# Kernel optimization log

Hardware: AMD Instinct MI355X
Metric: run time of the kernel (lower is better)

## Reference

```python
import jax, jax.numpy as jnp
import numpy as np

N = 200000   # nodes
E = 3200000  # edges
B = 1024     # graphs in batch
A = 10       # num_actions
IN, C, ED = 9, 64, 1
NEG_SLOPE = 0.2


def _xavier(k, shape):
    lim = (6.0 / (shape[0] + shape[1])) ** 0.5
    return jax.random.uniform(k, shape, jnp.float32, -lim, lim)


def setup_inputs() -> dict:
    key = jax.random.key(0)
    ks = jax.random.split(key, 24)
    x = jax.random.normal(ks[0], (N, IN), jnp.float32)
    edge_index = jax.random.randint(ks[1], (2, E), 0, N, dtype=jnp.int64)
    edge_attr = jax.random.normal(ks[2], (E, ED), jnp.float32)
    agent_state = jax.random.normal(ks[3], (B, 34), jnp.float32)
    pool_batch = jnp.sort(jax.random.randint(ks[4], (N,), 0, B, dtype=jnp.int64))
    return {
        "x": x, "edge_index": edge_index, "edge_attr": edge_attr,
        "agent_state": agent_state, "pool_batch": pool_batch,
        # GATConv params (heads=1): lin (no bias), lin_edge (no bias), att vectors, bias
        "W_gat": _xavier(ks[5], (IN, C)),
        "att_src": jax.random.normal(ks[6], (C,), jnp.float32) * 0.1,
        "att_dst": jax.random.normal(ks[7], (C,), jnp.float32) * 0.1,
        "W_edge": _xavier(ks[8], (ED, C)),
        "att_edge": jax.random.normal(ks[9], (C,), jnp.float32) * 0.1,
        "b_gat": jnp.zeros((C,), jnp.float32),
        # fc_input1: Linear(64,128)
        "W1": _xavier(ks[10], (C, 128)), "b1": jnp.zeros((128,), jnp.float32),
        # fc_input2: Linear(34,64)
        "W2": _xavier(ks[11], (34, 64)), "b2": jnp.zeros((64,), jnp.float32),
        # fc_output: Linear(192,128), Linear(128,A)
        "W3": _xavier(ks[12], (192, 128)), "b3": jnp.zeros((128,), jnp.float32),
        "W4": _xavier(ks[13], (128, A)), "b4": jnp.zeros((A,), jnp.float32),
    }


def _gat_forward(x, edge_index, edge_attr, W_gat, att_src, att_dst, W_edge, att_edge, b_gat):
    src, dst = edge_index[0], edge_index[1]
    # add self-loops; self-loop edge_attr = mean of incoming edge_attr (PyG fill_value='mean')
    ones = jnp.ones((E,), jnp.float32)
    deg = jax.ops.segment_sum(ones, dst, num_segments=N)
    loop_attr = jax.ops.segment_sum(edge_attr, dst, num_segments=N) / jnp.maximum(deg, 1.0)[:, None]
    loop_idx = jnp.arange(N, dtype=src.dtype)
    src_f = jnp.concatenate([src, loop_idx])
    dst_f = jnp.concatenate([dst, loop_idx])
    attr_f = jnp.concatenate([edge_attr, loop_attr], axis=0)  # [E+N, 1]
    h = x @ W_gat                                   # [N, C]
    a_src = h @ att_src                             # [N]
    a_dst = h @ att_dst                             # [N]
    a_edge = (attr_f @ W_edge) @ att_edge           # [E+N]
    alpha = jax.nn.leaky_relu(a_src[src_f] + a_dst[dst_f] + a_edge, NEG_SLOPE)
    # per-destination softmax (stable)
    m = jax.ops.segment_max(alpha, dst_f, num_segments=N)
    ea = jnp.exp(alpha - m[dst_f])
    denom = jax.ops.segment_sum(ea, dst_f, num_segments=N)
    coef = ea / denom[dst_f]                        # [E+N]
    out = jax.ops.segment_sum(coef[:, None] * h[src_f], dst_f, num_segments=N)
    return out + b_gat


def reference(x, edge_index, edge_attr, agent_state, pool_batch,
              W_gat, att_src, att_dst, W_edge, att_edge, b_gat,
              W1, b1, W2, b2, W3, b3, W4, b4):
    g = _gat_forward(x, edge_index, edge_attr, W_gat, att_src, att_dst, W_edge, att_edge, b_gat)
    g = jax.nn.relu(g @ W1 + b1)                    # [N, 128]
    # global mean pool per graph
    s = jax.ops.segment_sum(g, pool_batch, num_segments=B)
    cnt = jax.ops.segment_sum(jnp.ones((N,), g.dtype), pool_batch, num_segments=B)
    pooled = s / jnp.maximum(cnt, 1.0)[:, None]     # [B, 128]
    a = jax.nn.relu(agent_state @ W2 + b2)          # [B, 64]
    z = jnp.concatenate([pooled, a], axis=-1)       # [B, 192]
    z = jax.nn.relu(z @ W3 + b3)
    return z @ W4 + b4                              # [B, A]
```

## Files before the change

### kernel.cpp

```cpp
#include <hip/hip_runtime.h>
#include <hip/hip_bf16.h>

namespace {

constexpr int kN  = 200000;
constexpr int kE  = 3200000;
constexpr int kB  = 1024;
constexpr int kA  = 10;
constexpr int kIn = 9;
constexpr int kC  = 64;
constexpr int kH1 = 128;
constexpr int kAS = 34;
constexpr int kH2 = 64;
constexpr int kZ  = 192;
constexpr int kH3 = 128;
constexpr int kMAXD = 192;
constexpr int kGPB_MFMA = 10;
constexpr int kNBUCK = 782;
constexpr int kEPC  = 4096;
constexpr int kNCHK = (kE + kEPC - 1) / kEPC;

using bf16 = __hip_bfloat16;
typedef __attribute__((ext_vector_type(8))) short short8;
typedef __attribute__((ext_vector_type(4))) float f32x4;

__device__ __forceinline__ float b2f(bf16 v) { return __bfloat162float(v); }
__device__ __forceinline__ float lrelu(float x) { return x > 0.f ? x : 0.2f * x; }

__device__ __forceinline__ float ldf(const void* p, size_t i, int f32) {
  return f32 ? ((const float*)p)[i] : __bfloat162float(((const bf16*)p)[i]);
}
__device__ __forceinline__ int ldi(const void* p, size_t i, int i64) {
  return i64 ? (int)(((const long long*)p)[i]) : ((const int*)p)[i];
}

__global__ void k_init(const void* __restrict__ ei, const void* __restrict__ x,
                       const void* __restrict__ We, const void* __restrict__ ae,
                       const void* __restrict__ Wg, const void* __restrict__ vsw,
                       const void* __restrict__ vdw,
                       int* __restrict__ flags, float* __restrict__ scal) {
  __shared__ int c0, c1;
  int t = threadIdx.x;
  if (t == 0) { c0 = 0; c1 = 0; }
  __syncthreads();
  int zc = (((const int*)ei)[2 * t + 1] == 0) ? 1 : 0;
  int nc = 0;
  for (int j = t; j < 8192; j += 1024) {
    unsigned short u = ((const unsigned short*)x)[j];
    if ((u & 0x7F80u) == 0x7F80u) nc++;
  }
  atomicAdd(&c0, zc);
  atomicAdd(&c1, nc);
  __syncthreads();
  int f32 = (c1 > 3) ? 1 : 0;
  if (t == 0) { flags[0] = (c0 > 512) ? 1 : 0; flags[1] = f32; }
  int wid = t >> 6, lane = t & 63;
  if (wid == 0) {
    float p = ldf(We, lane, f32) * ldf(ae, lane, f32);
    #pragma unroll
    for (int o = 32; o > 0; o >>= 1) p += __shfl_xor(p, o);
    if (lane == 0) scal[0] = p;
  } else if (wid <= kIn) {
    int k = wid - 1;
    float w = ldf(Wg, (size_t)k * kC + lane, f32);
    float ps = w * ldf(vsw, lane, f32);
    float pd = w * ldf(vdw, lane, f32);
    #pragma unroll
    for (int o = 32; o > 0; o >>= 1) { ps += __shfl_xor(ps, o); pd += __shfl_xor(pd, o); }
    if (lane == 0) { scal[1 + k] = ps; scal[10 + k] = pd; }
  }
}

__global__ void k_prep(const void* __restrict__ W1, const void* __restrict__ b1,
                       const void* __restrict__ bgat, const int* __restrict__ flags,
                       short* __restrict__ w1t, float* __restrict__ bb1) {
  int f32 = flags[1];
  int tid = threadIdx.x;
  for (int i = tid; i < kC * kH1; i += 256) {
    int c = i >> 6, k = i & 63;
    float v = ldf(W1, (size_t)k * kH1 + c, f32);
    w1t[i] = (short)__bfloat16_as_ushort(__float2bfloat16(v));
  }
  if (tid < kH1) {
    int c = tid;
    float s = ldf(b1, c, f32);
    for (int k = 0; k < kC; ++k)
      s += ldf(bgat, k, f32) * ldf(W1, (size_t)k * kH1 + c, f32);
    bb1[c] = s;
  }
}

__global__ void k_diag(const int* __restrict__ flags, float ws_mb,
                       float* __restrict__ out) {
  int i = blockIdx.x * 256 + threadIdx.x;
  if (i >= kB * kA) return;
  float v;
  if (flags) v = (1 + flags[0]) * 1e7f + (1 + flags[1]) * 1e6f + fminf(ws_mb, 999999.f);
  else       v = 3e7f + fminf(ws_mb, 999999.f);
  out[i] = v;
}


__global__ void __launch_bounds__(256) r_hist(const void* __restrict__ ei,
                                              const int* __restrict__ flags,
                                              int* __restrict__ blockhist) {
  __shared__ int h[kNBUCK];
  int i64 = flags[0];
  int c = blockIdx.x, tid = threadIdx.x;
  for (int i = tid; i < kNBUCK; i += 256) h[i] = 0;
  __syncthreads();
  int e0 = c * kEPC;
  #pragma unroll
  for (int j = 0; j < 16; ++j) {
    int e = e0 + j * 256 + tid;
    if (e < kE) {
      int d = ldi(ei, (size_t)kE + e, i64);
      atomicAdd(&h[d >> 8], 1);
    }
  }
  __syncthreads();
  for (int i = tid; i < kNBUCK; i += 256) blockhist[(size_t)i * kNCHK + c] = h[i];
}

__global__ void __launch_bounds__(256) r_scanA(int* __restrict__ blockhist,
                                               int* __restrict__ buckettot) {
  __shared__ int lds[256];
  int b = blockIdx.x, tid = threadIdx.x;
  int run = 0;
  for (int c0 = 0; c0 < kNCHK; c0 += 256) {
    int idx = c0 + tid;
    int v = (idx < kNCHK) ? blockhist[(size_t)b * kNCHK + idx] : 0;
    int xv = v;
    lds[tid] = xv;
    __syncthreads();
    #pragma unroll
    for (int o = 1; o < 256; o <<= 1) {
      int t = (tid >= o) ? lds[tid - o] : 0;
      __syncthreads();
      xv += t;
      lds[tid] = xv;
      __syncthreads();
    }
    if (idx < kNCHK) blockhist[(size_t)b * kNCHK + idx] = run + xv - v;
    run += lds[255];
    __syncthreads();
  }
  if (tid == 0) buckettot[b] = run;
}

__global__ void r_scanB(const int* __restrict__ buckettot, int* __restrict__ bucketbase) {
  __shared__ int lds[1024];
  int tid = threadIdx.x;
  int v = (tid < kNBUCK) ? buckettot[tid] : 0;
  int xv = v;
  lds[tid] = xv;
  __syncthreads();
  #pragma unroll
  for (int o = 1; o < 1024; o <<= 1) {
    int t = (tid >= o) ? lds[tid - o] : 0;
    __syncthreads();
    xv += t;
    lds[tid] = xv;
    __syncthreads();
  }
  if (tid < kNBUCK) bucketbase[tid] = xv - v;
  if (tid == kNBUCK - 1) bucketbase[kNBUCK] = xv;
}

__global__ void __launch_bounds__(256) r_scatter(
    const void* __restrict__ ei, const void* __restrict__ eattr,
    const int* __restrict__ flags, const float* __restrict__ a_src,
    const float* __restrict__ scal, const int* __restrict__ blockhist,
    const int* __restrict__ bucketbase, int2* __restrict__ mid) {
  __shared__ int cur[kNBUCK];
  int i64 = flags[0], f32 = flags[1];
  int c = blockIdx.x, tid = threadIdx.x;
  for (int i = tid; i < kNBUCK; i += 256)
    cur[i] = bucketbase[i] + blockhist[(size_t)i * kNCHK + c];
  __syncthreads();
  float sedge = scal[0];
  int e0 = c * kEPC;
  #pragma unroll
  for (int j = 0; j < 16; ++j) {
    int e = e0 + j * 256 + tid;
    if (e < kE) {
      int s = ldi(ei, e, i64);
      int d = ldi(ei, (size_t)kE + e, i64);
      float ap = a_src[s] + sedge * ldf(eattr, e, f32);
      int pos = atomicAdd(&cur[d >> 8], 1);
      mid[pos] = make_int2(s | ((d & 255) << 18), __float_as_int(ap));
    }
  }
}

__global__ void __launch_bounds__(256) r_bucket(
    const int2* __restrict__ mid, const int* __restrict__ bucketbase,
    int* __restrict__ offs, int2* __restrict__ csr) {
  __shared__ int h[256], cur[256], lds[256];
  int b = blockIdx.x, tid = threadIdx.x;
  int base = bucketbase[b];
  int cnt = bucketbase[b + 1] - base;
  h[tid] = 0;
  __syncthreads();
  for (int i = tid; i < cnt; i += 256)
    atomicAdd(&h[(mid[base + i].x >> 18) & 255], 1);
  __syncthreads();
  int v = h[tid];
  int xv = v;
  lds[tid] = xv;
  __syncthreads();
  #pragma unroll
  for (int o = 1; o < 256; o <<= 1) {
    int t = (tid >= o) ? lds[tid - o] : 0;
    __syncthreads();
    xv += t;
    lds[tid] = xv;
    __syncthreads();
  }
  int excl = xv - v;
  int n = b * 256 + tid;
  if (n < kN) offs[n] = base + excl;
  if (b == kNBUCK - 1 && tid == 0) offs[kN] = kE;
  cur[tid] = excl;
  __syncthreads();
  for (int i = tid; i < cnt; i += 256) {
    int2 e = mid[base + i];
    int dl = (e.x >> 18) & 255;
    int pos = atomicAdd(&cur[dl], 1);
    csr[base + pos] = make_int2(e.x & 0x3FFFF, e.y);
  }
}


__global__ void k_asrc(const void* __restrict__ x, const int* __restrict__ flags,
                       const float* __restrict__ scal, float* __restrict__ a_src,
                       float* __restrict__ a_dst) {
  int n = blockIdx.x * 256 + threadIdx.x;
  if (n >= kN) return;
  int f32 = flags[1];
  float as_ = 0.f, ad_ = 0.f;
  #pragma unroll
  for (int k = 0; k < kIn; ++k) {
    float xv = ldf(x, (size_t)n * kIn + k, f32);
    as_ += xv * scal[1 + k];
    ad_ += xv * scal[10 + k];
  }
  a_src[n] = as_;
  a_dst[n] = ad_;
}

__global__ void k_node_h(const void* __restrict__ x, const void* __restrict__ Wg,
                         const int* __restrict__ flags, bf16* __restrict__ hout) {
  __shared__ float wg[kIn * kC];
  int f32 = flags[1];
  int tid = threadIdx.x;
  for (int i = tid; i < kIn * kC; i += 256) wg[i] = ldf(Wg, i, f32);
  __syncthreads();
  int n = blockIdx.x * 4 + (tid >> 6);
  int lane = tid & 63;
  float hc = 0.f;
  #pragma unroll
  for (int k = 0; k < kIn; ++k) hc += ldf(x, (size_t)n * kIn + k, f32) * wg[k * kC + lane];
  hout[(size_t)n * kC + lane] = __float2bfloat16(hc);
}

__global__ void __launch_bounds__(256) k_gather5(
    const bf16* __restrict__ h, const float* __restrict__ a_src,
    const float* __restrict__ a_dst, const int* __restrict__ offs,
    const int2* __restrict__ csr, bf16* __restrict__ gbuf) {
  int wid = threadIdx.x >> 6, lane = threadIdx.x & 63;
  int n0 = (blockIdx.x * 4 + wid) * 4;
  for (int t = 0; t < 4; ++t) {
    int n = n0 + t;
    int base = offs[n];
    int degc = min(offs[n + 1] - base, kMAXD);
    float adst = a_dst[n], asrcn = a_src[n];
    int s0_ = 0, s1_ = 0, s2_ = 0;
    float e0_ = 0.f, e1_ = 0.f, e2_ = 0.f;
    float sap = 0.f;
    if (lane < degc) {
      int2 c = csr[base + lane];
      s0_ = c.x;
      float ap = __int_as_float(c.y);
      sap += ap - a_src[s0_];
      e0_ = __expf(fminf(lrelu(ap + adst), 60.f));
    }
    if (lane + 64 < degc) {
      int2 c = csr[base + lane + 64];
      s1_ = c.x;
      float ap = __int_as_float(c.y);
      sap += ap - a_src[s1_];
      e1_ = __expf(fminf(lrelu(ap + adst), 60.f));
    }
    if (lane + 128 < degc) {
      int2 c = csr[base + lane + 128];
      s2_ = c.x;
      float ap = __int_as_float(c.y);
      sap += ap - a_src[s2_];
      e2_ = __expf(fminf(lrelu(ap + adst), 60.f));
    }
    float se = e0_ + e1_ + e2_;
    #pragma unroll
    for (int o = 32; o > 0; o >>= 1) {
      se  += __shfl_xor(se, o);
      sap += __shfl_xor(sap, o);
    }
    float la = sap / fmaxf((float)degc, 1.0f);
    float aself = lrelu(asrcn + adst + la);
    float eself = __expf(fminf(aself, 60.f));
    float inv = 1.f / (se + eself);
    float g = eself * b2f(h[(size_t)n * kC + lane]);
    int lim = min(degc, 64);
    int j = 0;
    for (; j + 3 < lim; j += 4) {
      int sa = __shfl(s0_, j),     sb = __shfl(s0_, j + 1);
      int sc = __shfl(s0_, j + 2), sd = __shfl(s0_, j + 3);
      float ea = __shfl(e0_, j),     eb = __shfl(e0_, j + 1);
      float ec = __shfl(e0_, j + 2), ed = __shfl(e0_, j + 3);
      float ha = b2f(h[(size_t)sa * kC + lane]);
      float hb = b2f(h[(size_t)sb * kC + lane]);
      float hcv = b2f(h[(size_t)sc * kC + lane]);
      float hd = b2f(h[(size_t)sd * kC + lane]);
      g += ea * ha;
      g += eb * hb;
      g += ec * hcv;
      g += ed * hd;
    }
    for (; j < lim; ++j)
      g += __shfl(e0_, j) * b2f(h[(size_t)__shfl(s0_, j) * kC + lane]);
    if (degc > 64) {
      int lim1 = min(degc, 128) - 64;
      for (int j2 = 0; j2 < lim1; ++j2)
        g += __shfl(e1_, j2) * b2f(h[(size_t)__shfl(s1_, j2) * kC + lane]);
      if (degc > 128) {
        int lim2 = degc - 128;
        for (int j2 = 0; j2 < lim2; ++j2)
          g += __shfl(e2_, j2) * b2f(h[(size_t)__shfl(s2_, j2) * kC + lane]);
      }
    }
    gbuf[(size_t)n * kC + lane] = __float2bfloat16(g * inv);
  }
}

__global__ void __launch_bounds__(512) k_fc1mfma(
    const short* __restrict__ gbuf, const short* __restrict__ w1t,
    const float* __restrict__ bb1, const void* __restrict__ pb,
    const int* __restrict__ flags, float* __restrict__ pooled) {
  int i64 = flags[0];
  int wv = threadIdx.x >> 6, lane = threadIdx.x & 63;
  int col = lane & 15, kg = lane >> 4;
  int c = wv * 16 + col;
  short8 bf0 = *(const short8*)(w1t + (size_t)c * kC + kg * 8);
  short8 bf1 = *(const short8*)(w1t + (size_t)c * kC + 32 + kg * 8);
  float bias = bb1[c];
  int curb = -1;
  float pacc = 0.f;
  int g0 = blockIdx.x * kGPB_MFMA;
  for (int gi = 0; gi < kGPB_MFMA; ++gi) {
    int n0 = (g0 + gi) * 16;
    const short* arow = gbuf + (size_t)(n0 + col) * kC + kg * 8;
    short8 a0 = *(const short8*)(arow);
    short8 a1 = *(const short8*)(arow + 32);
    f32x4 acc = {bias, bias, bias, bias};
    acc = __builtin_amdgcn_mfma_f32_16x16x32_bf16(a0, bf0, acc, 0, 0, 0);
    acc = __builtin_amdgcn_mfma_f32_16x16x32_bf16(a1, bf1, acc, 0, 0, 0);
    #pragma unroll
    for (int r = 0; r < 4; ++r) {
      int node = n0 + kg * 4 + r;
      int b = ldi(pb, node, i64);
      float v = fmaxf(acc[r], 0.f);
      if (b != curb) {
        if (curb >= 0) atomicAdd(pooled + (size_t)curb * kH1 + c, pacc);
        curb = b;
        pacc = 0.f;
      }
      pacc += v;
    }
  }
  if (curb >= 0) atomicAdd(pooled + (size_t)curb * kH1 + c, pacc);
}

__device__ __forceinline__ int lowb(const void* pb, int i64, int target) {
  int lo = 0, hi = kN;
  while (lo < hi) {
    int mid = (lo + hi) >> 1;
    if (ldi(pb, mid, i64) < target) lo = mid + 1; else hi = mid;
  }
  return lo;
}

__global__ void k_final(const float* __restrict__ pooled, const void* __restrict__ pb,
                        const void* __restrict__ agent, const void* __restrict__ W2,
                        const void* __restrict__ b2v, const void* __restrict__ W3,
                        const void* __restrict__ b3v, const void* __restrict__ W4,
                        const void* __restrict__ b4v, const int* __restrict__ flags,
                        float* __restrict__ out) {
  __shared__ float z[kZ];
  __shared__ float t[kH3];
  int i64 = flags[0], f32 = flags[1];
  int b = blockIdx.x, l = threadIdx.x;
  int c0 = lowb(pb, i64, b);
  int c1 = lowb(pb, i64, b + 1);
  float ct = fmaxf((float)(c1 - c0), 1.0f);
  float av = ldf(b2v, l, f32);
  for (int k = 0; k < kAS; ++k)
    av += ldf(agent, (size_t)b * kAS + k, f32) * ldf(W2, (size_t)k * kH2 + l, f32);
  z[kH1 + l] = fmaxf(av, 0.f);
  z[l] = pooled[(size_t)b * kH1 + l] / ct;
  z[64 + l] = pooled[(size_t)b * kH1 + 64 + l] / ct;
  __syncthreads();
  float t0 = ldf(b3v, l, f32), t1 = ldf(b3v, 64 + l, f32);
  for (int k = 0; k < kZ; ++k) {
    float zk = z[k];
    t0 += zk * ldf(W3, (size_t)k * kH3 + l, f32);
    t1 += zk * ldf(W3, (size_t)k * kH3 + 64 + l, f32);
  }
  t[l] = fmaxf(t0, 0.f);
  t[64 + l] = fmaxf(t1, 0.f);
  __syncthreads();
  if (l < kA) {
    float o = ldf(b4v, l, f32);
    for (int k = 0; k < kH3; ++k) o += t[k] * ldf(W4, (size_t)k * kA + l, f32);
    out[b * kA + l] = o;
  }
}

}

extern "C" void kernel_launch(void* const* d_in, const int* in_sizes, int n_in,
                              void* d_out, int out_size, void* d_ws, size_t ws_size,
                              hipStream_t stream) {
  const void* x     = d_in[0];
  const void* ei    = d_in[1];
  const void* eattr = d_in[2];
  const void* agent = d_in[3];
  const void* pb    = d_in[4];
  const void* Wg    = d_in[5];
  const void* att_s = d_in[6];
  const void* att_d = d_in[7];
  const void* We    = d_in[8];
  const void* att_e = d_in[9];
  const void* bgat  = d_in[10];
  const void* W1    = d_in[11];
  const void* b1    = d_in[12];
  const void* W2    = d_in[13];
  const void* b2v   = d_in[14];
  const void* W3    = d_in[15];
  const void* b3v   = d_in[16];
  const void* W4    = d_in[17];
  const void* b4v   = d_in[18];
  float* out = (float*)d_out;

  char* ws = (char*)d_ws;
  size_t off = 0;
  auto alloc = [&](size_t bytes) -> void* {
    void* p = ws + off;
    off += (bytes + 255) & ~size_t(255);
    return p;
  };
  int*   flags  = (int*)alloc(256);
  float* pooled = (float*)alloc(size_t(kB) * kH1 * 4);
  size_t zbytes = off;
  int*   offs      = (int*)alloc((size_t(kN) + 1) * 4);
  float* a_src     = (float*)alloc(size_t(kN) * 4);
  float* a_dst     = (float*)alloc(size_t(kN) * 4);
  float* scal      = (float*)alloc(256);
  short* w1t       = (short*)alloc(size_t(kC) * kH1 * 2);
  float* bb1       = (float*)alloc(size_t(kH1) * 4);
  int*   blockhist = (int*)alloc(size_t(kNBUCK) * kNCHK * 4);
  int*   buckettot = (int*)alloc(size_t(kNBUCK) * 4);
  int*   bucketbase= (int*)alloc((size_t(kNBUCK) + 1) * 4);
  int2*  csr       = (int2*)alloc(size_t(kE) * 8);
  bf16*  h         = (bf16*)alloc(size_t(kN) * kC * 2);
  char*  uni  = (char*)alloc(size_t(kE) * 8);
  int2*  mid  = (int2*)uni;
  bf16*  gbuf = (bf16*)uni;
  size_t need = off;

  float ws_mb = (float)(double(ws_size) / (1024.0 * 1024.0));

  if (ws_size < 4096) {
    k_diag<<<(kB * kA + 255) / 256, 256, 0, stream>>>(nullptr, ws_mb, out);
    return;
  }
  hipMemsetAsync(ws, 0, (ws_size < need) ? size_t(256) : zbytes, stream);
  k_init<<<1, 1024, 0, stream>>>(ei, x, We, att_e, Wg, att_s, att_d, flags, scal);
  if (ws_size < need) {
    k_diag<<<(kB * kA + 255) / 256, 256, 0, stream>>>(flags, ws_mb, out);
    return;
  }

  k_prep<<<1, 256, 0, stream>>>(W1, b1, bgat, flags, w1t, bb1);
  k_asrc<<<(kN + 255) / 256, 256, 0, stream>>>(x, flags, scal, a_src, a_dst);
  k_node_h<<<kN / 4, 256, 0, stream>>>(x, Wg, flags, h);
  r_hist<<<kNCHK, 256, 0, stream>>>(ei, flags, blockhist);
  r_scanA<<<kNBUCK, 256, 0, stream>>>(blockhist, buckettot);
  r_scanB<<<1, 1024, 0, stream>>>(buckettot, bucketbase);
  r_scatter<<<kNCHK, 256, 0, stream>>>(ei, eattr, flags, a_src, scal, blockhist,
                                       bucketbase, mid);
  r_bucket<<<kNBUCK, 256, 0, stream>>>(mid, bucketbase, offs, csr);
  k_gather5<<<kN / 16, 256, 0, stream>>>(h, a_src, a_dst, offs, csr, gbuf);
  k_fc1mfma<<<kN / (16 * kGPB_MFMA), 512, 0, stream>>>((const short*)gbuf, w1t, bb1,
                                                       pb, flags, pooled);
  k_final<<<kB, 64, 0, stream>>>(pooled, pb, agent, W2, b2v, W3, b3v, W4, b4v,
                                 flags, out);
}
```

Before: 393.9 us.

## Replace CSR build and per-node gather with bucket-local LDS atomic aggregation

Drops the second-level counting sort (r_bucket) and the CSR-based k_gather5. A new kernel processes each 128-node destination bucket directly from the partially sorted edge list, accumulating softmax denominators and weighted features with shared-memory atomics. It also fuses k_prep into k_init, and fuses node projection, attention scalars and the edge histogram into one launch. The aim is to save a full pass writing and reading the 3.2M-edge CSR and several launches, at the cost of contended LDS float atomics, one wave per edge in the gather loop, and accumulation order that is no longer deterministic.

```diff
diff --git a/kernel.cpp b/kernel.cpp
--- a/kernel.cpp
+++ b/kernel.cpp
@@ -14,11 +14,12 @@
 constexpr int kH2 = 64;
 constexpr int kZ  = 192;
 constexpr int kH3 = 128;
-constexpr int kMAXD = 192;
 constexpr int kGPB_MFMA = 10;
-constexpr int kNBUCK = 782;
+constexpr int kDB = 128;
+constexpr int kNBUCK2 = (kN + kDB - 1) / kDB;
 constexpr int kEPC  = 4096;
 constexpr int kNCHK = (kE + kEPC - 1) / kEPC;
+constexpr int kNODEBLK = kN / 4;
 
 using bf16 = __hip_bfloat16;
 typedef __attribute__((ext_vector_type(8))) short short8;
@@ -34,11 +35,13 @@
   return i64 ? (int)(((const long long*)p)[i]) : ((const int*)p)[i];
 }
 
-__global__ void k_init(const void* __restrict__ ei, const void* __restrict__ x,
-                       const void* __restrict__ We, const void* __restrict__ ae,
-                       const void* __restrict__ Wg, const void* __restrict__ vsw,
-                       const void* __restrict__ vdw,
-                       int* __restrict__ flags, float* __restrict__ scal) {
+__global__ void k_init2(const void* __restrict__ ei, const void* __restrict__ x,
+                        const void* __restrict__ We, const void* __restrict__ ae,
+                        const void* __restrict__ Wg, const void* __restrict__ vsw,
+                        const void* __restrict__ vdw, const void* __restrict__ W1,
+                        const void* __restrict__ b1, const void* __restrict__ bgat,
+                        int* __restrict__ flags, float* __restrict__ scal,
+                        short* __restrict__ w1t, float* __restrict__ bb1) {
   __shared__ int c0, c1;
   int t = threadIdx.x;
   if (t == 0) { c0 = 0; c1 = 0; }
@@ -69,20 +72,13 @@
     for (int o = 32; o > 0; o >>= 1) { ps += __shfl_xor(ps, o); pd += __shfl_xor(pd, o); }
     if (lane == 0) { scal[1 + k] = ps; scal[10 + k] = pd; }
   }
-}
-
-__global__ void k_prep(const void* __restrict__ W1, const void* __restrict__ b1,
-                       const void* __restrict__ bgat, const int* __restrict__ flags,
-                       short* __restrict__ w1t, float* __restrict__ bb1) {
-  int f32 = flags[1];
-  int tid = threadIdx.x;
-  for (int i = tid; i < kC * kH1; i += 256) {
+  for (int i = t; i < kC * kH1; i += 1024) {
     int c = i >> 6, k = i & 63;
     float v = ldf(W1, (size_t)k * kH1 + c, f32);
     w1t[i] = (short)__bfloat16_as_ushort(__float2bfloat16(v));
   }
-  if (tid < kH1) {
-    int c = tid;
+  if (t < kH1) {
+    int c = t;
     float s = ldf(b1, c, f32);
     for (int k = 0; k < kC; ++k)
       s += ldf(bgat, k, f32) * ldf(W1, (size_t)k * kH1 + c, f32);
@@ -100,26 +96,50 @@
   out[i] = v;
 }
 
-
-__global__ void __launch_bounds__(256) r_hist(const void* __restrict__ ei,
-                                              const int* __restrict__ flags,
-                                              int* __restrict__ blockhist) {
-  __shared__ int h[kNBUCK];
-  int i64 = flags[0];
-  int c = blockIdx.x, tid = threadIdx.x;
-  for (int i = tid; i < kNBUCK; i += 256) h[i] = 0;
-  __syncthreads();
-  int e0 = c * kEPC;
-  #pragma unroll
-  for (int j = 0; j < 16; ++j) {
-    int e = e0 + j * 256 + tid;
-    if (e < kE) {
-      int d = ldi(ei, (size_t)kE + e, i64);
-      atomicAdd(&h[d >> 8], 1);
+__global__ void __launch_bounds__(256) k_nodehist(
+    const void* __restrict__ x, const void* __restrict__ Wg,
+    const void* __restrict__ ei, const int* __restrict__ flags,
+    const float* __restrict__ scal, bf16* __restrict__ hout,
+    float* __restrict__ a_src, float* __restrict__ a_dst,
+    int* __restrict__ blockhist) {
+  int tid = threadIdx.x;
+  int f32 = flags[1];
+  if (blockIdx.x < kNODEBLK) {
+    __shared__ float wg[kIn * kC];
+    __shared__ float sc[19];
+    for (int i = tid; i < kIn * kC; i += 256) wg[i] = ldf(Wg, i, f32);
+    if (tid < 19) sc[tid] = scal[tid];
+    __syncthreads();
+    int n = blockIdx.x * 4 + (tid >> 6);
+    int lane = tid & 63;
+    float hc = 0.f, as_ = 0.f, ad_ = 0.f;
+    #pragma unroll
+    for (int k = 0; k < kIn; ++k) {
+      float xv = ldf(x, (size_t)n * kIn + k, f32);
+      hc  += xv * wg[k * kC + lane];
+      as_ += xv * sc[1 + k];
+      ad_ += xv * sc[10 + k];
     }
-  }
-  __syncthreads();
-  for (int i = tid; i < kNBUCK; i += 256) blockhist[(size_t)i * kNCHK + c] = h[i];
+    hout[(size_t)n * kC + lane] = __float2bfloat16(hc);
+    if (lane == 0) { a_src[n] = as_; a_dst[n] = ad_; }
+  } else {
+    __shared__ int hh[kNBUCK2];
+    int i64 = flags[0];
+    int c = blockIdx.x - kNODEBLK;
+    for (int i = tid; i < kNBUCK2; i += 256) hh[i] = 0;
+    __syncthreads();
+    int e0 = c * kEPC;
+    #pragma unroll
+    for (int j = 0; j < 16; ++j) {
+      int e = e0 + j * 256 + tid;
+      if (e < kE) {
+        int d = ldi(ei, (size_t)kE + e, i64);
+        atomicAdd(&hh[d >> 7], 1);
+      }
+    }
+    __syncthreads();
+    for (int i = tid; i < kNBUCK2; i += 256) blockhist[(size_t)i * kNCHK + c] = hh[i];
+  }
 }
 
 __global__ void __launch_bounds__(256) r_scanA(int* __restrict__ blockhist,
@@ -151,8 +171,11 @@
 __global__ void r_scanB(const int* __restrict__ buckettot, int* __restrict__ bucketbase) {
   __shared__ int lds[1024];
   int tid = threadIdx.x;
-  int v = (tid < kNBUCK) ? buckettot[tid] : 0;
-  int xv = v;
+  int i0 = tid * 2, i1 = tid * 2 + 1;
+  int v0 = (i0 < kNBUCK2) ? buckettot[i0] : 0;
+  int v1 = (i1 < kNBUCK2) ? buckettot[i1] : 0;
+  int s = v0 + v1;
+  int xv = s;
   lds[tid] = xv;
   __syncthreads();
   #pragma unroll
@@ -163,8 +186,10 @@
     lds[tid] = xv;
     __syncthreads();
   }
-  if (tid < kNBUCK) bucketbase[tid] = xv - v;
-  if (tid == kNBUCK - 1) bucketbase[kNBUCK] = xv;
+  int excl = xv - s;
+  if (i0 < kNBUCK2) bucketbase[i0] = excl;
+  if (i1 < kNBUCK2) bucketbase[i1] = excl + v0;
+  if (tid == 1023) bucketbase[kNBUCK2] = xv;
 }
 
 __global__ void __launch_bounds__(256) r_scatter(
@@ -172,10 +197,10 @@
     const int* __restrict__ flags, const float* __restrict__ a_src,
     const float* __restrict__ scal, const int* __restrict__ blockhist,
     const int* __restrict__ bucketbase, int2* __restrict__ mid) {
-  __shared__ int cur[kNBUCK];
+  __shared__ int cur[kNBUCK2];
   int i64 = flags[0], f32 = flags[1];
   int c = blockIdx.x, tid = threadIdx.x;
-  for (int i = tid; i < kNBUCK; i += 256)
+  for (int i = tid; i < kNBUCK2; i += 256)
     cur[i] = bucketbase[i] + blockhist[(size_t)i * kNCHK + c];
   __syncthreads();
   float sedge = scal[0];
@@ -187,158 +212,56 @@
       int s = ldi(ei, e, i64);
       int d = ldi(ei, (size_t)kE + e, i64);
       float ap = a_src[s] + sedge * ldf(eattr, e, f32);
-      int pos = atomicAdd(&cur[d >> 8], 1);
-      mid[pos] = make_int2(s | ((d & 255) << 18), __float_as_int(ap));
+      int pos = atomicAdd(&cur[d >> 7], 1);
+      mid[pos] = make_int2(s | ((d & 127) << 18), __float_as_int(ap));
     }
   }
 }
 
-__global__ void __launch_bounds__(256) r_bucket(
+__global__ void __launch_bounds__(256) k_bucketgather(
     const int2* __restrict__ mid, const int* __restrict__ bucketbase,
-    int* __restrict__ offs, int2* __restrict__ csr) {
-  __shared__ int h[256], cur[256], lds[256];
+    const float* __restrict__ a_src, const float* __restrict__ a_dst,
+    const bf16* __restrict__ h, bf16* __restrict__ gbuf) {
+  __shared__ float acc[kDB][65];
+  __shared__ float denom[kDB], sap[kDB];
+  __shared__ int dcnt[kDB];
   int b = blockIdx.x, tid = threadIdx.x;
   int base = bucketbase[b];
-  int cnt = bucketbase[b + 1] - base;
-  h[tid] = 0;
-  __syncthreads();
-  for (int i = tid; i < cnt; i += 256)
-    atomicAdd(&h[(mid[base + i].x >> 18) & 255], 1);
-  __syncthreads();
-  int v = h[tid];
-  int xv = v;
-  lds[tid] = xv;
-  __syncthreads();
-  #pragma unroll
-  for (int o = 1; o < 256; o <<= 1) {
-    int t = (tid >= o) ? lds[tid - o] : 0;
-    __syncthreads();
-    xv += t;
-    lds[tid] = xv;
-    __syncthreads();
-  }
-  int excl = xv - v;
-  int n = b * 256 + tid;
-  if (n < kN) offs[n] = base + excl;
-  if (b == kNBUCK - 1 && tid == 0) offs[kN] = kE;
-  cur[tid] = excl;
+  int cnt  = bucketbase[b + 1] - base;
+  int n0 = b * kDB;
+  for (int i = tid; i < kDB * 65; i += 256) (&acc[0][0])[i] = 0.f;
+  if (tid < kDB) { denom[tid] = 0.f; sap[tid] = 0.f; dcnt[tid] = 0; }
   __syncthreads();
   for (int i = tid; i < cnt; i += 256) {
     int2 e = mid[base + i];
-    int dl = (e.x >> 18) & 255;
-    int pos = atomicAdd(&cur[dl], 1);
-    csr[base + pos] = make_int2(e.x & 0x3FFFF, e.y);
-  }
-}
-
-
-__global__ void k_asrc(const void* __restrict__ x, const int* __restrict__ flags,
-                       const float* __restrict__ scal, float* __restrict__ a_src,
-                       float* __restrict__ a_dst) {
-  int n = blockIdx.x * 256 + threadIdx.x;
-  if (n >= kN) return;
-  int f32 = flags[1];
-  float as_ = 0.f, ad_ = 0.f;
-  #pragma unroll
-  for (int k = 0; k < kIn; ++k) {
-    float xv = ldf(x, (size_t)n * kIn + k, f32);
-    as_ += xv * scal[1 + k];
-    ad_ += xv * scal[10 + k];
-  }
-  a_src[n] = as_;
-  a_dst[n] = ad_;
-}
-
-__global__ void k_node_h(const void* __restrict__ x, const void* __restrict__ Wg,
-                         const int* __restrict__ flags, bf16* __restrict__ hout) {
-  __shared__ float wg[kIn * kC];
-  int f32 = flags[1];
-  int tid = threadIdx.x;
-  for (int i = tid; i < kIn * kC; i += 256) wg[i] = ldf(Wg, i, f32);
-  __syncthreads();
-  int n = blockIdx.x * 4 + (tid >> 6);
-  int lane = tid & 63;
-  float hc = 0.f;
-  #pragma unroll
-  for (int k = 0; k < kIn; ++k) hc += ldf(x, (size_t)n * kIn + k, f32) * wg[k * kC + lane];
-  hout[(size_t)n * kC + lane] = __float2bfloat16(hc);
-}
-
-__global__ void __launch_bounds__(256) k_gather5(
-    const bf16* __restrict__ h, const float* __restrict__ a_src,
-    const float* __restrict__ a_dst, const int* __restrict__ offs,
-    const int2* __restrict__ csr, bf16* __restrict__ gbuf) {
-  int wid = threadIdx.x >> 6, lane = threadIdx.x & 63;
-  int n0 = (blockIdx.x * 4 + wid) * 4;
-  for (int t = 0; t < 4; ++t) {
-    int n = n0 + t;
-    int base = offs[n];
-    int degc = min(offs[n + 1] - base, kMAXD);
-    float adst = a_dst[n], asrcn = a_src[n];
-    int s0_ = 0, s1_ = 0, s2_ = 0;
-    float e0_ = 0.f, e1_ = 0.f, e2_ = 0.f;
-    float sap = 0.f;
-    if (lane < degc) {
-      int2 c = csr[base + lane];
-      s0_ = c.x;
-      float ap = __int_as_float(c.y);
-      sap += ap - a_src[s0_];
-      e0_ = __expf(fminf(lrelu(ap + adst), 60.f));
-    }
-    if (lane + 64 < degc) {
-      int2 c = csr[base + lane + 64];
-      s1_ = c.x;
-      float ap = __int_as_float(c.y);
-      sap += ap - a_src[s1_];
-      e1_ = __expf(fminf(lrelu(ap + adst), 60.f));
-    }
-    if (lane + 128 < degc) {
-      int2 c = csr[base + lane + 128];
-      s2_ = c.x;
-      float ap = __int_as_float(c.y);
-      sap += ap - a_src[s2_];
-      e2_ = __expf(fminf(lrelu(ap + adst), 60.f));
-    }
-    float se = e0_ + e1_ + e2_;
-    #pragma unroll
-    for (int o = 32; o > 0; o >>= 1) {
-      se  += __shfl_xor(se, o);
-      sap += __shfl_xor(sap, o);
-    }
-    float la = sap / fmaxf((float)degc, 1.0f);
-    float aself = lrelu(asrcn + adst + la);
+    int s  = e.x & 0x3FFFF;
+    int dl = (e.x >> 18) & (kDB - 1);
+    float ap = __int_as_float(e.y);
+    float coef = __expf(fminf(lrelu(ap + a_dst[n0 + dl]), 60.f));
+    atomicAdd(&denom[dl], coef);
+    atomicAdd(&sap[dl], ap - a_src[s]);
+    atomicAdd(&dcnt[dl], 1);
+  }
+  __syncthreads();
+  int wid = tid >> 6, lane = tid & 63;
+  for (int i = wid; i < cnt; i += 4) {
+    int2 e = mid[base + i];
+    int s  = e.x & 0x3FFFF;
+    int dl = (e.x >> 18) & (kDB - 1);
+    float coef = __expf(fminf(lrelu(__int_as_float(e.y) + a_dst[n0 + dl]), 60.f));
+    float hv = b2f(h[(size_t)s * kC + lane]);
+    atomicAdd(&acc[dl][lane], coef * hv);
+  }
+  __syncthreads();
+  for (int dl = wid; dl < kDB; dl += 4) {
+    int n = n0 + dl;
+    if (n >= kN) break;
+    float la = sap[dl] / fmaxf((float)dcnt[dl], 1.f);
+    float aself = lrelu(a_src[n] + a_dst[n] + la);
     float eself = __expf(fminf(aself, 60.f));
-    float inv = 1.f / (se + eself);
-    float g = eself * b2f(h[(size_t)n * kC + lane]);
-    int lim = min(degc, 64);
-    int j = 0;
-    for (; j + 3 < lim; j += 4) {
-      int sa = __shfl(s0_, j),     sb = __shfl(s0_, j + 1);
-      int sc = __shfl(s0_, j + 2), sd = __shfl(s0_, j + 3);
-      float ea = __shfl(e0_, j),     eb = __shfl(e0_, j + 1);
-      float ec = __shfl(e0_, j + 2), ed = __shfl(e0_, j + 3);
-      float ha = b2f(h[(size_t)sa * kC + lane]);
-      float hb = b2f(h[(size_t)sb * kC + lane]);
-      float hcv = b2f(h[(size_t)sc * kC + lane]);
-      float hd = b2f(h[(size_t)sd * kC + lane]);
-      g += ea * ha;
-      g += eb * hb;
-      g += ec * hcv;
-      g += ed * hd;
-    }
-    for (; j < lim; ++j)
-      g += __shfl(e0_, j) * b2f(h[(size_t)__shfl(s0_, j) * kC + lane]);
-    if (degc > 64) {
-      int lim1 = min(degc, 128) - 64;
-      for (int j2 = 0; j2 < lim1; ++j2)
-        g += __shfl(e1_, j2) * b2f(h[(size_t)__shfl(s1_, j2) * kC + lane]);
-      if (degc > 128) {
-        int lim2 = degc - 128;
-        for (int j2 = 0; j2 < lim2; ++j2)
-          g += __shfl(e2_, j2) * b2f(h[(size_t)__shfl(s2_, j2) * kC + lane]);
-      }
-    }
-    gbuf[(size_t)n * kC + lane] = __float2bfloat16(g * inv);
+    float inv = 1.f / (denom[dl] + eself);
+    float g = (acc[dl][lane] + eself * b2f(h[(size_t)n * kC + lane])) * inv;
+    gbuf[(size_t)n * kC + lane] = __float2bfloat16(g);
   }
 }
 
@@ -461,20 +384,18 @@
   int*   flags  = (int*)alloc(256);
   float* pooled = (float*)alloc(size_t(kB) * kH1 * 4);
   size_t zbytes = off;
-  int*   offs      = (int*)alloc((size_t(kN) + 1) * 4);
-  float* a_src     = (float*)alloc(size_t(kN) * 4);
-  float* a_dst     = (float*)alloc(size_t(kN) * 4);
-  float* scal      = (float*)alloc(256);
-  short* w1t       = (short*)alloc(size_t(kC) * kH1 * 2);
-  float* bb1       = (float*)alloc(size_t(kH1) * 4);
-  int*   blockhist = (int*)alloc(size_t(kNBUCK) * kNCHK * 4);
-  int*   buckettot = (int*)alloc(size_t(kNBUCK) * 4);
-  int*   bucketbase= (int*)alloc((size_t(kNBUCK) + 1) * 4);
-  int2*  csr       = (int2*)alloc(size_t(kE) * 8);
-  bf16*  h         = (bf16*)alloc(size_t(kN) * kC * 2);
-  char*  uni  = (char*)alloc(size_t(kE) * 8);
-  int2*  mid  = (int2*)uni;
-  bf16*  gbuf = (bf16*)uni;
+  float* scal       = (float*)alloc(256);
+  short* w1t        = (short*)alloc(size_t(kC) * kH1 * 2);
+  float* bb1        = (float*)alloc(size_t(kH1) * 4);
+  int*   buckettot  = (int*)alloc(size_t(kNBUCK2) * 4);
+  int*   bucketbase = (int*)alloc((size_t(kNBUCK2) + 1) * 4);
+  float* a_src      = (float*)alloc(size_t(kN) * 4);
+  float* a_dst      = (float*)alloc(size_t(kN) * 4);
+  bf16*  h   = (bf16*)alloc(size_t(kN) * kC * 2);
+  int2*  mid = (int2*)alloc(size_t(kE) * 8);
+  char*  uni = (char*)alloc(size_t(kN) * kC * 2);
+  int*   blockhist = (int*)uni;
+  bf16*  gbuf      = (bf16*)uni;
   size_t need = off;
 
   float ws_mb = (float)(double(ws_size) / (1024.0 * 1024.0));
@@ -484,22 +405,20 @@
     return;
   }
   hipMemsetAsync(ws, 0, (ws_size < need) ? size_t(256) : zbytes, stream);
-  k_init<<<1, 1024, 0, stream>>>(ei, x, We, att_e, Wg, att_s, att_d, flags, scal);
+  k_init2<<<1, 1024, 0, stream>>>(ei, x, We, att_e, Wg, att_s, att_d, W1, b1, bgat,
+                                  flags, scal, w1t, bb1);
   if (ws_size < need) {
     k_diag<<<(kB * kA + 255) / 256, 256, 0, stream>>>(flags, ws_mb, out);
     return;
   }
 
-  k_prep<<<1, 256, 0, stream>>>(W1, b1, bgat, flags, w1t, bb1);
-  k_asrc<<<(kN + 255) / 256, 256, 0, stream>>>(x, flags, scal, a_src, a_dst);
-  k_node_h<<<kN / 4, 256, 0, stream>>>(x, Wg, flags, h);
-  r_hist<<<kNCHK, 256, 0, stream>>>(ei, flags, blockhist);
-  r_scanA<<<kNBUCK, 256, 0, stream>>>(blockhist, buckettot);
+  k_nodehist<<<kNODEBLK + kNCHK, 256, 0, stream>>>(x, Wg, ei, flags, scal, h,
+                                                   a_src, a_dst, blockhist);
+  r_scanA<<<kNBUCK2, 256, 0, stream>>>(blockhist, buckettot);
   r_scanB<<<1, 1024, 0, stream>>>(buckettot, bucketbase);
   r_scatter<<<kNCHK, 256, 0, stream>>>(ei, eattr, flags, a_src, scal, blockhist,
                                        bucketbase, mid);
-  r_bucket<<<kNBUCK, 256, 0, stream>>>(mid, bucketbase, offs, csr);
-  k_gather5<<<kN / 16, 256, 0, stream>>>(h, a_src, a_dst, offs, csr, gbuf);
+  k_bucketgather<<<kNBUCK2, 256, 0, stream>>>(mid, bucketbase, a_src, a_dst, h, gbuf);
   k_fc1mfma<<<kN / (16 * kGPB_MFMA), 512, 0, stream>>>((const short*)gbuf, w1t, bb1,
                                                        pb, flags, pooled);
   k_final<<<kB, 64, 0, stream>>>(pooled, pb, agent, W2, b2v, W3, b3v, W4, b4v,
```

Result: slower. 1.539 ms (+290.8%).

## Merge setup kernels and fuse node projection, attention scores and edge histogram

Applied to the files above, without the earlier changes.

Folds the W1 transpose and bias prep into the single-block init kernel, and merges node-feature projection, per-node attention logits and the destination histogram into one launch whose blocks branch on index. This removes four launches and their serialization gaps, lets the histogram blocks overlap with node work, and reads x once for both h and a_src/a_dst. The cost is a larger, heterogeneous grid whose two block types use different shared-memory layouts, which may lower occupancy for the node blocks. The workspace buffers are also reordered.

```diff
diff --git a/kernel.cpp b/kernel.cpp
--- a/kernel.cpp
+++ b/kernel.cpp
@@ -19,6 +19,7 @@
 constexpr int kNBUCK = 782;
 constexpr int kEPC  = 4096;
 constexpr int kNCHK = (kE + kEPC - 1) / kEPC;
+constexpr int kNODEBLK = kN / 4;
 
 using bf16 = __hip_bfloat16;
 typedef __attribute__((ext_vector_type(8))) short short8;
@@ -34,11 +35,13 @@
   return i64 ? (int)(((const long long*)p)[i]) : ((const int*)p)[i];
 }
 
-__global__ void k_init(const void* __restrict__ ei, const void* __restrict__ x,
-                       const void* __restrict__ We, const void* __restrict__ ae,
-                       const void* __restrict__ Wg, const void* __restrict__ vsw,
-                       const void* __restrict__ vdw,
-                       int* __restrict__ flags, float* __restrict__ scal) {
+__global__ void k_init2(const void* __restrict__ ei, const void* __restrict__ x,
+                        const void* __restrict__ We, const void* __restrict__ ae,
+                        const void* __restrict__ Wg, const void* __restrict__ vsw,
+                        const void* __restrict__ vdw, const void* __restrict__ W1,
+                        const void* __restrict__ b1, const void* __restrict__ bgat,
+                        int* __restrict__ flags, float* __restrict__ scal,
+                        short* __restrict__ w1t, float* __restrict__ bb1) {
   __shared__ int c0, c1;
   int t = threadIdx.x;
   if (t == 0) { c0 = 0; c1 = 0; }
@@ -69,20 +72,13 @@
     for (int o = 32; o > 0; o >>= 1) { ps += __shfl_xor(ps, o); pd += __shfl_xor(pd, o); }
     if (lane == 0) { scal[1 + k] = ps; scal[10 + k] = pd; }
   }
-}
-
-__global__ void k_prep(const void* __restrict__ W1, const void* __restrict__ b1,
-                       const void* __restrict__ bgat, const int* __restrict__ flags,
-                       short* __restrict__ w1t, float* __restrict__ bb1) {
-  int f32 = flags[1];
-  int tid = threadIdx.x;
-  for (int i = tid; i < kC * kH1; i += 256) {
+  for (int i = t; i < kC * kH1; i += 1024) {
     int c = i >> 6, k = i & 63;
     float v = ldf(W1, (size_t)k * kH1 + c, f32);
     w1t[i] = (short)__bfloat16_as_ushort(__float2bfloat16(v));
   }
-  if (tid < kH1) {
-    int c = tid;
+  if (t < kH1) {
+    int c = t;
     float s = ldf(b1, c, f32);
     for (int k = 0; k < kC; ++k)
       s += ldf(bgat, k, f32) * ldf(W1, (size_t)k * kH1 + c, f32);
@@ -100,26 +96,50 @@
   out[i] = v;
 }
 
-
-__global__ void __launch_bounds__(256) r_hist(const void* __restrict__ ei,
-                                              const int* __restrict__ flags,
-                                              int* __restrict__ blockhist) {
-  __shared__ int h[kNBUCK];
-  int i64 = flags[0];
-  int c = blockIdx.x, tid = threadIdx.x;
-  for (int i = tid; i < kNBUCK; i += 256) h[i] = 0;
-  __syncthreads();
-  int e0 = c * kEPC;
-  #pragma unroll
-  for (int j = 0; j < 16; ++j) {
-    int e = e0 + j * 256 + tid;
-    if (e < kE) {
-      int d = ldi(ei, (size_t)kE + e, i64);
-      atomicAdd(&h[d >> 8], 1);
-    }
-  }
-  __syncthreads();
-  for (int i = tid; i < kNBUCK; i += 256) blockhist[(size_t)i * kNCHK + c] = h[i];
+__global__ void __launch_bounds__(256) k_nodehist(
+    const void* __restrict__ x, const void* __restrict__ Wg,
+    const void* __restrict__ ei, const int* __restrict__ flags,
+    const float* __restrict__ scal, bf16* __restrict__ hout,
+    float* __restrict__ a_src, float* __restrict__ a_dst,
+    int* __restrict__ blockhist) {
+  int tid = threadIdx.x;
+  int f32 = flags[1];
+  if (blockIdx.x < kNODEBLK) {
+    __shared__ float wg[kIn * kC];
+    __shared__ float sc[19];
+    for (int i = tid; i < kIn * kC; i += 256) wg[i] = ldf(Wg, i, f32);
+    if (tid < 19) sc[tid] = scal[tid];
+    __syncthreads();
+    int n = blockIdx.x * 4 + (tid >> 6);
+    int lane = tid & 63;
+    float hc = 0.f, as_ = 0.f, ad_ = 0.f;
+    #pragma unroll
+    for (int k = 0; k < kIn; ++k) {
+      float xv = ldf(x, (size_t)n * kIn + k, f32);
+      hc  += xv * wg[k * kC + lane];
+      as_ += xv * sc[1 + k];
+      ad_ += xv * sc[10 + k];
+    }
+    hout[(size_t)n * kC + lane] = __float2bfloat16(hc);
+    if (lane == 0) { a_src[n] = as_; a_dst[n] = ad_; }
+  } else {
+    __shared__ int hh[kNBUCK];
+    int i64 = flags[0];
+    int c = blockIdx.x - kNODEBLK;
+    for (int i = tid; i < kNBUCK; i += 256) hh[i] = 0;
+    __syncthreads();
+    int e0 = c * kEPC;
+    #pragma unroll
+    for (int j = 0; j < 16; ++j) {
+      int e = e0 + j * 256 + tid;
+      if (e < kE) {
+        int d = ldi(ei, (size_t)kE + e, i64);
+        atomicAdd(&hh[d >> 8], 1);
+      }
+    }
+    __syncthreads();
+    for (int i = tid; i < kNBUCK; i += 256) blockhist[(size_t)i * kNCHK + c] = hh[i];
+  }
 }
 
 __global__ void __launch_bounds__(256) r_scanA(int* __restrict__ blockhist,
@@ -229,39 +249,6 @@
     int pos = atomicAdd(&cur[dl], 1);
     csr[base + pos] = make_int2(e.x & 0x3FFFF, e.y);
   }
-}
-
-
-__global__ void k_asrc(const void* __restrict__ x, const int* __restrict__ flags,
-                       const float* __restrict__ scal, float* __restrict__ a_src,
-                       float* __restrict__ a_dst) {
-  int n = blockIdx.x * 256 + threadIdx.x;
-  if (n >= kN) return;
-  int f32 = flags[1];
-  float as_ = 0.f, ad_ = 0.f;
-  #pragma unroll
-  for (int k = 0; k < kIn; ++k) {
-    float xv = ldf(x, (size_t)n * kIn + k, f32);
-    as_ += xv * scal[1 + k];
-    ad_ += xv * scal[10 + k];
-  }
-  a_src[n] = as_;
-  a_dst[n] = ad_;
-}
-
-__global__ void k_node_h(const void* __restrict__ x, const void* __restrict__ Wg,
-                         const int* __restrict__ flags, bf16* __restrict__ hout) {
-  __shared__ float wg[kIn * kC];
-  int f32 = flags[1];
-  int tid = threadIdx.x;
-  for (int i = tid; i < kIn * kC; i += 256) wg[i] = ldf(Wg, i, f32);
-  __syncthreads();
-  int n = blockIdx.x * 4 + (tid >> 6);
-  int lane = tid & 63;
-  float hc = 0.f;
-  #pragma unroll
-  for (int k = 0; k < kIn; ++k) hc += ldf(x, (size_t)n * kIn + k, f32) * wg[k * kC + lane];
-  hout[(size_t)n * kC + lane] = __float2bfloat16(hc);
 }
 
 __global__ void __launch_bounds__(256) k_gather5(
@@ -461,17 +448,17 @@
   int*   flags  = (int*)alloc(256);
   float* pooled = (float*)alloc(size_t(kB) * kH1 * 4);
   size_t zbytes = off;
-  int*   offs      = (int*)alloc((size_t(kN) + 1) * 4);
-  float* a_src     = (float*)alloc(size_t(kN) * 4);
-  float* a_dst     = (float*)alloc(size_t(kN) * 4);
-  float* scal      = (float*)alloc(256);
-  short* w1t       = (short*)alloc(size_t(kC) * kH1 * 2);
-  float* bb1       = (float*)alloc(size_t(kH1) * 4);
-  int*   blockhist = (int*)alloc(size_t(kNBUCK) * kNCHK * 4);
-  int*   buckettot = (int*)alloc(size_t(kNBUCK) * 4);
-  int*   bucketbase= (int*)alloc((size_t(kNBUCK) + 1) * 4);
-  int2*  csr       = (int2*)alloc(size_t(kE) * 8);
-  bf16*  h         = (bf16*)alloc(size_t(kN) * kC * 2);
+  float* scal       = (float*)alloc(256);
+  short* w1t        = (short*)alloc(size_t(kC) * kH1 * 2);
+  float* bb1        = (float*)alloc(size_t(kH1) * 4);
+  int*   buckettot  = (int*)alloc(size_t(kNBUCK) * 4);
+  int*   bucketbase = (int*)alloc((size_t(kNBUCK) + 1) * 4);
+  float* a_src      = (float*)alloc(size_t(kN) * 4);
+  float* a_dst      = (float*)alloc(size_t(kN) * 4);
+  int*   offs       = (int*)alloc((size_t(kN) + 1) * 4);
+  int*   blockhist  = (int*)alloc(size_t(kNBUCK) * kNCHK * 4);
+  int2*  csr = (int2*)alloc(size_t(kE) * 8);
+  bf16*  h   = (bf16*)alloc(size_t(kN) * kC * 2);
   char*  uni  = (char*)alloc(size_t(kE) * 8);
   int2*  mid  = (int2*)uni;
   bf16*  gbuf = (bf16*)uni;
@@ -484,16 +471,15 @@
     return;
   }
   hipMemsetAsync(ws, 0, (ws_size < need) ? size_t(256) : zbytes, stream);
-  k_init<<<1, 1024, 0, stream>>>(ei, x, We, att_e, Wg, att_s, att_d, flags, scal);
+  k_init2<<<1, 1024, 0, stream>>>(ei, x, We, att_e, Wg, att_s, att_d, W1, b1, bgat,
+                                  flags, scal, w1t, bb1);
   if (ws_size < need) {
     k_diag<<<(kB * kA + 255) / 256, 256, 0, stream>>>(flags, ws_mb, out);
     return;
   }
 
-  k_prep<<<1, 256, 0, stream>>>(W1, b1, bgat, flags, w1t, bb1);
-  k_asrc<<<(kN + 255) / 256, 256, 0, stream>>>(x, flags, scal, a_src, a_dst);
-  k_node_h<<<kN / 4, 256, 0, stream>>>(x, Wg, flags, h);
-  r_hist<<<kNCHK, 256, 0, stream>>>(ei, flags, blockhist);
+  k_nodehist<<<kNODEBLK + kNCHK, 256, 0, stream>>>(x, Wg, ei, flags, scal, h,
+                                                   a_src, a_dst, blockhist);
   r_scanA<<<kNBUCK, 256, 0, stream>>>(blockhist, buckettot);
   r_scanB<<<1, 1024, 0, stream>>>(buckettot, bucketbase);
   r_scatter<<<kNCHK, 256, 0, stream>>>(ei, eattr, flags, a_src, scal, blockhist,
```

Measured after the change: 392.3 us. Within noise of the previous version (-0.4%).
